# Kernel optimization log

Hardware: AMD Instinct MI355X
Metric: run time of the kernel (lower is better)

The kernel has to match this reference:

```python
import jax, jax.numpy as jnp
import numpy as np

K = 10
NEG_SLOPE = 0.2


def _knn(x, k):
    # x: (B, C, N) -> idx (B, N, k) of k nearest neighbors (smallest sq-dist)
    inner = -2.0 * jnp.einsum('bcn,bcm->bnm', x, x)
    xx = jnp.sum(x * x, axis=1)  # (B, N)
    pd = -xx[:, :, None] - inner - xx[:, None, :]  # negative squared distance
    return jax.lax.top_k(pd, k)[1]


def _gather(xt, idx):
    # xt: (B, N, C), idx: (B, N, k) -> (B, N, k, C)
    return jax.vmap(lambda f, i: f[i])(xt, idx)


def graph_feature(x, k):
    # x: (B, C, N) -> (B, 2C, N, k)
    idx = _knn(x, k)
    xt = jnp.transpose(x, (0, 2, 1))  # (B, N, C)
    feat = _gather(xt, idx)           # (B, N, k, C)
    xc = xt[:, :, None, :]
    out = jnp.concatenate([feat - xc, jnp.broadcast_to(xc, feat.shape)], axis=3)
    return jnp.transpose(out, (0, 3, 1, 2))


def graph_feature1(x, k):
    # knn on first 2 dims (2D coords); x: (B, C, N) -> (B, 2C, N, k)
    idx = _knn(x[:, 0:2, :], k)
    xt = jnp.transpose(x, (0, 2, 1))
    feat = _gather(xt, idx)
    xc = jnp.broadcast_to(xt[:, :, None, :], feat.shape)
    out = jnp.concatenate([feat[..., :2] - xc[..., :2], feat[..., 2:], xc], axis=3)
    return jnp.transpose(out, (0, 3, 1, 2))


def _lrelu(v):
    return jnp.where(v >= 0, v, NEG_SLOPE * v)


def _cbr2(f, W, s, t):
    # 1x1 conv2d + folded-BN + leaky relu; f: (B, C, N, k)
    y = jnp.einsum('oc,bcnk->bonk', W, f)
    return _lrelu(y * s[None, :, None, None] + t[None, :, None, None])


def _cbr1(f, W, s, t):
    # 1x1 conv1d + folded-BN + leaky relu; f: (B, C, N)
    y = jnp.einsum('oc,bcn->bon', W, f)
    return _lrelu(y * s[None, :, None] + t[None, :, None])


def setup_inputs() -> dict:
    key = jax.random.key(0)
    ks = jax.random.split(key, 32)
    B, C, N = 8, 7, 4096
    d = {'x': jax.random.normal(ks[0], (B, C, N), jnp.float32)}
    wshapes = [('W1', (64, 14)), ('W2', (64, 64)), ('W3', (64, 128)), ('W4', (64, 64)),
               ('W5', (64, 128)), ('W6', (256, 192)), ('W7', (512, 448)), ('W8', (128, 1024))]
    for i, (n, s) in enumerate(wshapes):
        d[n] = jax.random.normal(ks[1 + i], s, jnp.float32) * (1.0 / np.sqrt(s[1]))
    bdims = [64, 64, 64, 64, 64, 256, 512, 128]
    for i, c in enumerate(bdims):
        d[f's{i + 1}'] = jax.random.uniform(ks[9 + i], (c,), jnp.float32, 0.5, 1.5)
        d[f't{i + 1}'] = jax.random.normal(ks[17 + i], (c,), jnp.float32) * 0.1
    return d


def reference(x, W1, W2, W3, W4, W5, W6, W7, W8,
              s1, s2, s3, s4, s5, s6, s7, s8,
              t1, t2, t3, t4, t5, t6, t7, t8):
    B, _, N = x.shape
    h = graph_feature1(x, K)              # (B, 14, N, K)
    h = _cbr2(h, W1, s1, t1)
    h = _cbr2(h, W2, s2, t2)
    x1 = h.mean(axis=-1)                  # (B, 64, N)
    h = graph_feature(x1, K)              # (B, 128, N, K)
    h = _cbr2(h, W3, s3, t3)
    h = _cbr2(h, W4, s4, t4)
    x2 = h.mean(axis=-1)
    h = graph_feature(x2, K)
    h = _cbr2(h, W5, s5, t5)
    x3 = h.mean(axis=-1)
    h = jnp.concatenate([x1, x2, x3], axis=1)   # (B, 192, N)
    h = _cbr1(h, W6, s6, t6)                    # (B, 256, N)
    g = h.mean(axis=-1, keepdims=True)          # (B, 256, 1)
    g = jnp.broadcast_to(g, (B, 256, N))
    h = jnp.concatenate([g, x1, x2, x3], axis=1)  # (B, 448, N)
    h = _cbr1(h, W7, s7, t7)                      # (B, 512, N)
    x4 = h.max(axis=-1)
    x5 = h.mean(axis=-1)
    h = jnp.concatenate([x4, x5], axis=1)         # (B, 1024)
    h = h @ W8.T                                  # (B, 128)
    return _lrelu(h * s8[None, :] + t8[None, :])
```

## Files before the change

### kernel.cpp

```cpp
#include <hip/hip_runtime.h>

#define BB 8
#define NN 4096
#define KK 10
#define CAP 24
#define TT 4
typedef unsigned long long u64;
typedef __attribute__((ext_vector_type(8))) short bf16x8;
typedef __attribute__((ext_vector_type(4))) float f32x4;

__device__ __forceinline__ float lrelu(float v){ return v >= 0.f ? v : 0.2f*v; }
__device__ __forceinline__ float bc(float v, int l){
  return __int_as_float(__builtin_amdgcn_readlane(__float_as_int(v), l));
}
__device__ __forceinline__ unsigned fenc(float f){
  unsigned u = __float_as_uint(f);
  return u ^ (((unsigned)((int)u >> 31)) | 0x80000000u);
}
__device__ __forceinline__ float fdec(unsigned e){
  return (e & 0x80000000u) ? __uint_as_float(e & 0x7fffffffu) : __uint_as_float(~e);
}

__global__ __launch_bounds__(256) void prep_k(
    const float* __restrict__ W1, const float* __restrict__ W2, const float* __restrict__ W3,
    const float* __restrict__ W4, const float* __restrict__ W5, const float* __restrict__ W8,
    float* __restrict__ W1T, float* __restrict__ W2T, float* __restrict__ W8T,
    unsigned short* __restrict__ W3dh, unsigned short* __restrict__ W3dl,
    unsigned short* __restrict__ W3qh, unsigned short* __restrict__ W3ql,
    unsigned short* __restrict__ W4h,  unsigned short* __restrict__ W4l,
    unsigned short* __restrict__ W5dh, unsigned short* __restrict__ W5dl,
    unsigned short* __restrict__ W5qh, unsigned short* __restrict__ W5ql)
{
  const int t = blockIdx.x*256 + threadIdx.x;
  const int stride = gridDim.x*256;
  for (int i=t; i<64*14; i+=stride){ int o=i/14, c=i%14; W1T[c*64+o]=W1[i]; }
  for (int i=t; i<64*64; i+=stride){ int o=i>>6, c=i&63; W2T[c*64+o]=W2[i]; }
  for (int i=t; i<128*1024; i+=stride){ int o=i>>10, c=i&1023; W8T[c*128+o]=W8[i]; }
  for (int i=t; i<64*64; i+=stride){
    int o=i>>6, c=i&63;
    float f = W3[o*128 + c];
    unsigned u = __float_as_uint(f);
    W3dh[i] = (unsigned short)(u >> 16);
    float lo = f - __uint_as_float(u & 0xffff0000u);
    W3dl[i] = (unsigned short)(__float_as_uint(lo) >> 16);
  }
  for (int i=t; i<64*64; i+=stride){
    int o=i>>6, c=i&63;
    float f = W3[o*128 + 64 + c];
    unsigned u = __float_as_uint(f);
    W3qh[i] = (unsigned short)(u >> 16);
    float lo = f - __uint_as_float(u & 0xffff0000u);
    W3ql[i] = (unsigned short)(__float_as_uint(lo) >> 16);
  }
  for (int i=t; i<64*64; i+=stride){
    float f = W4[i];
    unsigned u = __float_as_uint(f);
    W4h[i] = (unsigned short)(u >> 16);
    float lo = f - __uint_as_float(u & 0xffff0000u);
    W4l[i] = (unsigned short)(__float_as_uint(lo) >> 16);
  }
  for (int i=t; i<64*64; i+=stride){
    int o=i>>6, c=i&63;
    float f = W5[o*128 + c];
    unsigned u = __float_as_uint(f);
    W5dh[i] = (unsigned short)(u >> 16);
    float lo = f - __uint_as_float(u & 0xffff0000u);
    W5dl[i] = (unsigned short)(__float_as_uint(lo) >> 16);
  }
  for (int i=t; i<64*64; i+=stride){
    int o=i>>6, c=i&63;
    float f = W5[o*128 + 64 + c];
    unsigned u = __float_as_uint(f);
    W5qh[i] = (unsigned short)(u >> 16);
    float lo = f - __uint_as_float(u & 0xffff0000u);
    W5ql[i] = (unsigned short)(__float_as_uint(lo) >> 16);
  }
}

__global__ __launch_bounds__(256) void cvt_k(const float* __restrict__ xin,
    unsigned short* __restrict__ Xh, unsigned short* __restrict__ Xl, float* __restrict__ xx)
{
  const int gid = blockIdx.x*256 + threadIdx.x;
  const int p = gid >> 3, c8 = (gid & 7) << 3;
  const float* src = xin + (size_t)p*64 + c8;
  float fv[8];
  *(float4*)&fv[0] = *(const float4*)(src);
  *(float4*)&fv[4] = *(const float4*)(src + 4);
  unsigned hp[4], lp[4];
  float ssq = 0.f;
  #pragma unroll
  for (int e=0; e<4; e++){
    float f0 = fv[2*e], f1 = fv[2*e+1];
    ssq += f0*f0 + f1*f1;
    unsigned u0 = __float_as_uint(f0), u1 = __float_as_uint(f1);
    hp[e] = (u0 >> 16) | (u1 & 0xffff0000u);
    float l0 = f0 - __uint_as_float(u0 & 0xffff0000u);
    float l1 = f1 - __uint_as_float(u1 & 0xffff0000u);
    lp[e] = (__float_as_uint(l0) >> 16) | (__float_as_uint(l1) & 0xffff0000u);
  }
  *(uint4*)(Xh + (size_t)p*64 + c8) = uint4{hp[0],hp[1],hp[2],hp[3]};
  *(uint4*)(Xl + (size_t)p*64 + c8) = uint4{lp[0],lp[1],lp[2],lp[3]};
  ssq += __shfl_xor(ssq, 1, 64);
  ssq += __shfl_xor(ssq, 2, 64);
  ssq += __shfl_xor(ssq, 4, 64);
  if ((gid & 7) == 0) xx[p] = ssq;
}

__global__ __launch_bounds__(256) void knn2d_k(const float* __restrict__ x, u64* __restrict__ pk)
{
  __shared__ float px[1024], py[1024], pxx[1024];
  __shared__ unsigned cnt[64];
  __shared__ u64 lst[CAP][64];
  const int tid = threadIdx.x;
  const int b  = blockIdx.x >> 8;
  const int qt = (blockIdx.x >> 2) & 63;
  const int h  = blockIdx.x & 3;
  const int q0 = qt*64;
  const int m0g = h*1024;
  const float* xb = x + (size_t)b*7*NN;
  for (int m = tid; m < 1024; m += 256){
    float a = xb[m0g + m], c = xb[NN + m0g + m];
    px[m] = a; py[m] = c; pxx[m] = a*a + c*c;
  }
  if (tid < 64) cnt[tid] = 0;
  __syncthreads();

  const int ty = tid >> 4, tx = tid & 15;
  const int qr = ty*4;
  float qx4[4], qy4[4], q24[4];
  #pragma unroll
  for (int i=0;i<4;i++){
    float a = xb[q0+qr+i], c = xb[NN + q0+qr+i];
    qx4[i] = a; qy4[i] = c; q24[i] = a*a + c*c;
  }

  float bv[4][TT];
  #pragma unroll
  for (int i=0;i<4;i++){
    #pragma unroll
    for (int s=0;s<TT;s++) bv[i][s] = -__builtin_inff();
  }

  for (int ot=0; ot<8; ot++){
    #pragma unroll
    for (int j=0;j<8;j++){
      const int ml = ot*128 + j*16 + tx;
      const float cmx = px[ml], cmy = py[ml], cm2 = pxx[ml];
      #pragma unroll
      for (int i=0;i<4;i++){
        float dot = qx4[i]*cmx + qy4[i]*cmy;
        float v = (-q24[i]) - (-2.f*dot) - cm2;
        float c = v;
        #pragma unroll
        for (int s=0;s<TT;s++){
          float nb = fmaxf(bv[i][s], c);
          c = fminf(bv[i][s], c);
          bv[i][s] = nb;
        }
      }
    }
  }

  float thr[4];
  #pragma unroll
  for (int i=0;i<4;i++){
    float m = 0.f;
    #pragma unroll
    for (int k=0;k<10;k++){
      float hh = bv[i][0];
      m = hh;
      m = fmaxf(m, __shfl_xor(m, 1, 64));
      m = fmaxf(m, __shfl_xor(m, 2, 64));
      m = fmaxf(m, __shfl_xor(m, 4, 64));
      m = fmaxf(m, __shfl_xor(m, 8, 64));
      if (k < 9){
        if (hh == m){
          #pragma unroll
          for (int s=0;s<TT-1;s++) bv[i][s] = bv[i][s+1];
          bv[i][TT-1] = -__builtin_inff();
        }
      }
    }
    thr[i] = m;
  }

  for (int ot=0; ot<8; ot++){
    #pragma unroll
    for (int j=0;j<8;j++){
      const int ml = ot*128 + j*16 + tx;
      const float cmx = px[ml], cmy = py[ml], cm2 = pxx[ml];
// ... 74 lines not shown
  }

  for (int ct=0; ct<16; ct++){
    const int m0 = m0g + ct*64;
    __syncthreads();
    {
      const uint4* sh = (const uint4*)(Xhb + (size_t)(m0+sp)*64 + sc);
      const uint4* sl = (const uint4*)(Xlb + (size_t)(m0+sp)*64 + sc);
      uint4 h0 = sh[0], h1 = sh[1], l0 = sl[0], l1 = sl[1];
      *(uint4*)(&Ch[sp*72 + sc])     = h0;
      *(uint4*)(&Ch[sp*72 + sc + 8]) = h1;
      *(uint4*)(&Cl[sp*72 + sc])     = l0;
      *(uint4*)(&Cl[sp*72 + sc + 8]) = l1;
      if (tid < 64) cxx[tid] = xxb[m0 + tid];
    }
    __syncthreads();

    #pragma unroll
    for (int j=0;j<4;j++){
      const int boff = (j*16 + col)*72 + quad*8;
      bf16x8 Bh0 = *(const bf16x8*)(&Ch[boff]);
      bf16x8 Bh1 = *(const bf16x8*)(&Ch[boff+32]);
      bf16x8 Bl0 = *(const bf16x8*)(&Cl[boff]);
      bf16x8 Bl1 = *(const bf16x8*)(&Cl[boff+32]);
      f32x4 d = {0.f,0.f,0.f,0.f};
      d = __builtin_amdgcn_mfma_f32_16x16x32_bf16(Al0, Bh0, d, 0,0,0);
      d = __builtin_amdgcn_mfma_f32_16x16x32_bf16(Ah0, Bl0, d, 0,0,0);
      d = __builtin_amdgcn_mfma_f32_16x16x32_bf16(Ah0, Bh0, d, 0,0,0);
      d = __builtin_amdgcn_mfma_f32_16x16x32_bf16(Al1, Bh1, d, 0,0,0);
      d = __builtin_amdgcn_mfma_f32_16x16x32_bf16(Ah1, Bl1, d, 0,0,0);
      d = __builtin_amdgcn_mfma_f32_16x16x32_bf16(Ah1, Bh1, d, 0,0,0);

      const float cx = cxx[j*16 + col];
      #pragma unroll
      for (int i=0;i<4;i++){
        float v = (-qx4[i]) - (-2.f*d[i]) - cx;
        float c = v;
        #pragma unroll
        for (int s=0;s<TT;s++){
          float nb = fmaxf(bv[i][s], c);
          c = fminf(bv[i][s], c);
          bv[i][s] = nb;
        }
      }
    }
  }

  float thr[4];
  #pragma unroll
  for (int i=0;i<4;i++){
    float m = 0.f;
    #pragma unroll
    for (int k=0;k<10;k++){
      float hh = bv[i][0];
      m = hh;
      m = fmaxf(m, __shfl_xor(m, 1, 64));
      m = fmaxf(m, __shfl_xor(m, 2, 64));
      m = fmaxf(m, __shfl_xor(m, 4, 64));
      m = fmaxf(m, __shfl_xor(m, 8, 64));
      if (k < 9){
        if (hh == m){
          #pragma unroll
          for (int s=0;s<TT-1;s++) bv[i][s] = bv[i][s+1];
          bv[i][TT-1] = -__builtin_inff();
        }
      }
    }
    thr[i] = m;
  }

  for (int ct=0; ct<16; ct++){
    const int m0 = m0g + ct*64;
    __syncthreads();
    {
      const uint4* sh = (const uint4*)(Xhb + (size_t)(m0+sp)*64 + sc);
      const uint4* sl = (const uint4*)(Xlb + (size_t)(m0+sp)*64 + sc);
      uint4 h0 = sh[0], h1 = sh[1], l0 = sl[0], l1 = sl[1];
      *(uint4*)(&Ch[sp*72 + sc])     = h0;
      *(uint4*)(&Ch[sp*72 + sc + 8]) = h1;
      *(uint4*)(&Cl[sp*72 + sc])     = l0;
      *(uint4*)(&Cl[sp*72 + sc + 8]) = l1;
      if (tid < 64) cxx[tid] = xxb[m0 + tid];
    }
    __syncthreads();

    #pragma unroll
    for (int j=0;j<4;j++){
      const int boff = (j*16 + col)*72 + quad*8;
      bf16x8 Bh0 = *(const bf16x8*)(&Ch[boff]);
      bf16x8 Bh1 = *(const bf16x8*)(&Ch[boff+32]);
      bf16x8 Bl0 = *(const bf16x8*)(&Cl[boff]);
      bf16x8 Bl1 = *(const bf16x8*)(&Cl[boff+32]);
      f32x4 d = {0.f,0.f,0.f,0.f};
      d = __builtin_amdgcn_mfma_f32_16x16x32_bf16(Al0, Bh0, d, 0,0,0);
      d = __builtin_amdgcn_mfma_f32_16x16x32_bf16(Ah0, Bl0, d, 0,0,0);
      d = __builtin_amdgcn_mfma_f32_16x16x32_bf16(Ah0, Bh0, d, 0,0,0);
      d = __builtin_amdgcn_mfma_f32_16x16x32_bf16(Al1, Bh1, d, 0,0,0);
      d = __builtin_amdgcn_mfma_f32_16x16x32_bf16(Ah1, Bl1, d, 0,0,0);
      d = __builtin_amdgcn_mfma_f32_16x16x32_bf16(Ah1, Bh1, d, 0,0,0);

      const int m = m0 + j*16 + col;
      const float cx = cxx[j*16 + col];
      const unsigned mk = ~(unsigned)m;
      #pragma unroll
      for (int i=0;i<4;i++){
        float v = (-qx4[i]) - (-2.f*d[i]) - cx;
        if (v >= thr[i]){
          u64 key = ((u64)fenc(v) << 32) | mk;
          const int r = qr + i;
          unsigned slot = atomicAdd(&cnt[r], 1u);
          if (slot < CAP) lst[slot][r] = key;
        }
      }
    }
  }
  __syncthreads();

  if (tid < 64){
    int n = (int)cnt[tid]; if (n > CAP) n = CAP;
    u64* op = pk + (((size_t)b*NN + q0 + tid)*4 + h)*KK;
    for (int k=0;k<KK;k++){
      u64 best = 0ull; int bi = 0;
      for (int s=0;s<n;s++){
        u64 v2 = lst[s][tid];
        if (v2 > best){ best = v2; bi = s; }
      }
      if (best) lst[bi][tid] = 0ull;
      op[k] = best;
    }
  }
}

__global__ __launch_bounds__(256) void kmerge_k(const u64* __restrict__ pk, int* __restrict__ idxo)
{
  const int q = blockIdx.x*256 + threadIdx.x;
  const u64* A = pk + (size_t)q*(4*KK);
  int* op = idxo + (size_t)q*KK;
  int ia = 0, ib = 0, ic = 0, id = 0;
  #pragma unroll
  for (int k=0;k<KK;k++){
    u64 a  = (ia < KK) ? A[ia]        : 0ull;
    u64 b2 = (ib < KK) ? A[KK + ib]   : 0ull;
    u64 c2 = (ic < KK) ? A[2*KK + ic] : 0ull;
    u64 d2 = (id < KK) ? A[3*KK + id] : 0ull;
    u64 m1 = a >= b2 ? a : b2;  int s1 = a >= b2 ? 0 : 1;
    u64 m2 = c2 >= d2 ? c2 : d2; int s2 = c2 >= d2 ? 2 : 3;
    u64 mm = m1 >= m2 ? m1 : m2; int ss = m1 >= m2 ? s1 : s2;
    op[k] = (int)(~(unsigned)mm);
    if (ss == 0) ia++; else if (ss == 1) ib++; else if (ss == 2) ic++; else id++;
  }
}

__global__ __launch_bounds__(256) void edge1_k(const float* __restrict__ x, const int* __restrict__ idx,
    const float* __restrict__ W1T, const float* __restrict__ W2T,
    const float* __restrict__ s1, const float* __restrict__ t1,
    const float* __restrict__ s2, const float* __restrict__ t2,
    float* __restrict__ x1t)
{
  const int lane = threadIdx.x & 63;
  const int pt = (blockIdx.x << 2) + (threadIdx.x >> 6);
  const int b = pt >> 12, n = pt & 4095;
  const float* xb = x + (size_t)b*7*NN;
  float w1r[14], w2r[64];
  #pragma unroll
  for (int c=0;c<14;c++) w1r[c] = W1T[c*64 + lane];
  #pragma unroll
  for (int c=0;c<64;c++) w2r[c] = W2T[c*64 + lane];
  const float s1o=s1[lane], t1o=t1[lane], s2o=s2[lane], t2o=t2[lane];
  const float xq = (lane < 7) ? xb[lane*NN + n] : 0.f;
  const float xq0 = bc(xq,0), xq1 = bc(xq,1);
  float qy1 = 0.f;
  #pragma unroll
  for (int c=0;c<7;c++) qy1 += w1r[7+c]*bc(xq,c);
  const int* ip = idx + (size_t)pt*KK;
  float acc = 0.f;
  for (int j=0;j<KK;j++){
    const int ij = ip[j];
    const float xg = (lane < 7) ? xb[lane*NN + ij] : 0.f;
    float y1 = qy1;
    y1 += w1r[0]*(bc(xg,0) - xq0);
    y1 += w1r[1]*(bc(xg,1) - xq1);
    #pragma unroll
    for (int c=2;c<7;c++) y1 += w1r[c]*bc(xg,c);
    const float z1 = lrelu(y1*s1o + t1o);
    float p0=0.f,p1=0.f,p2=0.f,p3=0.f;
    #pragma unroll
    for (int c=0;c<64;c+=4){
      p0 += w2r[c+0]*bc(z1,c+0);
      p1 += w2r[c+1]*bc(z1,c+1);
      p2 += w2r[c+2]*bc(z1,c+2);
      p3 += w2r[c+3]*bc(z1,c+3);
    }
    acc += lrelu(((p0+p1)+(p2+p3))*s2o + t2o);
  }
  x1t[(size_t)pt*64 + lane] = acc / 10.f;
}

__global__ __launch_bounds__(256) void edge2_k(const float* __restrict__ x1t, const int* __restrict__ idx,
    const unsigned short* __restrict__ W3dh, const unsigned short* __restrict__ W3dl,
    const unsigned short* __restrict__ W3qh, const unsigned short* __restrict__ W3ql,
    const unsigned short* __restrict__ W4h,  const unsigned short* __restrict__ W4l,
    const float* __restrict__ s3, const float* __restrict__ t3,
    const float* __restrict__ s4, const float* __restrict__ t4,
    float* __restrict__ xout)
{
  __shared__ unsigned short Zh[80*72], Zl[80*72];
  __shared__ unsigned short Qh[16*72], Ql[16*72];
  __shared__ float accf[64*8];
  const int tid = threadIdx.x;
  const size_t p0 = (size_t)blockIdx.x * 8;

  ((float2*)accf)[tid] = float2{0.f, 0.f};

  #pragma unroll
  for (int pass=0; pass<2; ++pass){
    const int col = pass*64 + (tid>>2);
    const int sc16 = (tid&3)*16;
    if (col < 88){
      float dv[16];
      if (col < 80){
        const int p = col/10, j = col - p*10;
        const size_t pt = p0 + p;
        const int bb = (int)(pt >> 12);
        const int ij = idx[pt*KK + j];
        const float* gs = x1t + ((size_t)bb*NN + ij)*64 + sc16;
        const float* qs = x1t + pt*64 + sc16;
        #pragma unroll
        for (int e=0;e<4;e++){
          float4 g4 = *(const float4*)(gs + e*4);
          float4 q4 = *(const float4*)(qs + e*4);
          dv[e*4+0]=g4.x-q4.x; dv[e*4+1]=g4.y-q4.y; dv[e*4+2]=g4.z-q4.z; dv[e*4+3]=g4.w-q4.w;
        }
      } else {
        const int cl = col - 80;
        const float* qs = x1t + (size_t)(p0+cl)*64 + sc16;
        #pragma unroll
        for (int e=0;e<4;e++){
          float4 q4 = *(const float4*)(qs + e*4);
          dv[e*4+0]=q4.x; dv[e*4+1]=q4.y; dv[e*4+2]=q4.z; dv[e*4+3]=q4.w;
        }
      }
      unsigned hp[8], lp[8];
      #pragma unroll
      for (int e=0;e<8;e++){
        float f0 = dv[2*e], f1 = dv[2*e+1];
        unsigned u0 = __float_as_uint(f0), u1 = __float_as_uint(f1);
        hp[e] = (u0 >> 16) | (u1 & 0xffff0000u);
        float l0 = f0 - __uint_as_float(u0 & 0xffff0000u);
        float l1 = f1 - __uint_as_float(u1 & 0xffff0000u);
        lp[e] = (__float_as_uint(l0) >> 16) | (__float_as_uint(l1) & 0xffff0000u);
      }
      if (col < 80){
        *(uint4*)(&Zh[col*72 + sc16])     = uint4{hp[0],hp[1],hp[2],hp[3]};
        *(uint4*)(&Zh[col*72 + sc16 + 8]) = uint4{hp[4],hp[5],hp[6],hp[7]};
        *(uint4*)(&Zl[col*72 + sc16])     = uint4{lp[0],lp[1],lp[2],lp[3]};
        *(uint4*)(&Zl[col*72 + sc16 + 8]) = uint4{lp[4],lp[5],lp[6],lp[7]};
      } else {
        const int cl = col - 80;
        *(uint4*)(&Qh[cl*72 + sc16])     = uint4{hp[0],hp[1],hp[2],hp[3]};
        *(uint4*)(&Qh[cl*72 + sc16 + 8]) = uint4{hp[4],hp[5],hp[6],hp[7]};
        *(uint4*)(&Ql[cl*72 + sc16])     = uint4{lp[0],lp[1],lp[2],lp[3]};
        *(uint4*)(&Ql[cl*72 + sc16 + 8]) = uint4{lp[4],lp[5],lp[6],lp[7]};
      }
    } else if (col < 96){
      const int cl = col - 80;
      const uint4 z{0u,0u,0u,0u};
      *(uint4*)(&Qh[cl*72 + sc16])     = z;
      *(uint4*)(&Qh[cl*72 + sc16 + 8]) = z;
      *(uint4*)(&Ql[cl*72 + sc16])     = z;
      *(uint4*)(&Ql[cl*72 + sc16 + 8]) = z;
    }
  }
  __syncthreads();

  const int lane = tid & 63;
  const int w    = tid >> 6;
  const int colL = lane & 15;
  const int quad = lane >> 4;
  const int arow = (w*16 + colL)*64 + quad*8;

  bf16x8 Adh0 = *(const bf16x8*)(W3dh + arow);
  bf16x8 Adh1 = *(const bf16x8*)(W3dh + arow + 32);
  bf16x8 Adl0 = *(const bf16x8*)(W3dl + arow);
  bf16x8 Adl1 = *(const bf16x8*)(W3dl + arow + 32);

  f32x4 C1[5];
  #pragma unroll
  for (int t=0;t<5;t++){
    const int boff = (t*16 + colL)*72 + quad*8;
    bf16x8 Bh0 = *(const bf16x8*)(&Zh[boff]);
    bf16x8 Bh1 = *(const bf16x8*)(&Zh[boff+32]);
    bf16x8 Bl0 = *(const bf16x8*)(&Zl[boff]);
    bf16x8 Bl1 = *(const bf16x8*)(&Zl[boff+32]);
    f32x4 d = {0.f,0.f,0.f,0.f};
    d = __builtin_amdgcn_mfma_f32_16x16x32_bf16(Adl0, Bh0, d, 0,0,0);
    d = __builtin_amdgcn_mfma_f32_16x16x32_bf16(Adh0, Bl0, d, 0,0,0);
    d = __builtin_amdgcn_mfma_f32_16x16x32_bf16(Adh0, Bh0, d, 0,0,0);
    d = __builtin_amdgcn_mfma_f32_16x16x32_bf16(Adl1, Bh1, d, 0,0,0);
    d = __builtin_amdgcn_mfma_f32_16x16x32_bf16(Adh1, Bl1, d, 0,0,0);
    d = __builtin_amdgcn_mfma_f32_16x16x32_bf16(Adh1, Bh1, d, 0,0,0);
    C1[t] = d;
  }
  f32x4 Cu;
  {
    bf16x8 Aqh0 = *(const bf16x8*)(W3qh + arow);
    bf16x8 Aqh1 = *(const bf16x8*)(W3qh + arow + 32);
    bf16x8 Aql0 = *(const bf16x8*)(W3ql + arow);
    bf16x8 Aql1 = *(const bf16x8*)(W3ql + arow + 32);
    const int boff = colL*72 + quad*8;
    bf16x8 Bh0 = *(const bf16x8*)(&Qh[boff]);
    bf16x8 Bh1 = *(const bf16x8*)(&Qh[boff+32]);
    bf16x8 Bl0 = *(const bf16x8*)(&Ql[boff]);
    bf16x8 Bl1 = *(const bf16x8*)(&Ql[boff+32]);
    f32x4 d = {0.f,0.f,0.f,0.f};
    d = __builtin_amdgcn_mfma_f32_16x16x32_bf16(Aql0, Bh0, d, 0,0,0);
    d = __builtin_amdgcn_mfma_f32_16x16x32_bf16(Aqh0, Bl0, d, 0,0,0);
    d = __builtin_amdgcn_mfma_f32_16x16x32_bf16(Aqh0, Bh0, d, 0,0,0);
    d = __builtin_amdgcn_mfma_f32_16x16x32_bf16(Aql1, Bh1, d, 0,0,0);
    d = __builtin_amdgcn_mfma_f32_16x16x32_bf16(Aqh1, Bl1, d, 0,0,0);
    d = __builtin_amdgcn_mfma_f32_16x16x32_bf16(Aqh1, Bh1, d, 0,0,0);
    Cu = d;
  }

  float s3v[4], t3v[4], s4v[4], t4v[4];
  #pragma unroll
  for (int i=0;i<4;i++){
    const int o = w*16 + quad*4 + i;
    s3v[i]=s3[o]; t3v[i]=t3[o]; s4v[i]=s4[o]; t4v[i]=t4[o];
  }

  __syncthreads();

  #pragma unroll
  for (int t=0;t<5;t++){
    const int gc = t*16 + colL;
    const int p  = gc/10;
    const int srcb = (((lane & 48) | p) << 2);
    float z[4];
    #pragma unroll
    for (int i=0;i<4;i++){
      float ui = __int_as_float(__builtin_amdgcn_ds_bpermute(srcb, __float_as_int(Cu[i])));
      float zp = (C1[t][i] + ui)*s3v[i] + t3v[i];
      z[i] = zp >= 0.f ? zp : 0.2f*zp;
    }
    unsigned u0=__float_as_uint(z[0]), u1=__float_as_uint(z[1]);
    unsigned u2=__float_as_uint(z[2]), u3=__float_as_uint(z[3]);
    unsigned h01 = (u0>>16) | (u1 & 0xffff0000u);
    unsigned h23 = (u2>>16) | (u3 & 0xffff0000u);
// ... 280 lines not shown
{
  const int b = blockIdx.x >> 1;
  const int o = (blockIdx.x & 1)*256 + threadIdx.x;
  const float* wr = W7 + (size_t)o*448;
  const float* gb = gsum + b*256;
  float a0=0.f,a1=0.f,a2=0.f,a3=0.f;
  #pragma unroll 4
  for (int c=0;c<256;c+=4){
    a0 += wr[c+0]*gb[c+0]; a1 += wr[c+1]*gb[c+1];
    a2 += wr[c+2]*gb[c+2]; a3 += wr[c+3]*gb[c+3];
  }
  c7[b*512+o] = ((a0+a1)+(a2+a3)) * (1.f/4096.f);
}

__global__ __launch_bounds__(256) void g3_k(const float* __restrict__ W7,
   const float* __restrict__ x1t, const float* __restrict__ x2t, const float* __restrict__ x3t,
   const float* __restrict__ c7, const float* __restrict__ s7, const float* __restrict__ t7,
   unsigned* __restrict__ x4e, float* __restrict__ x5s)
{
  __shared__ float Wl[16*132];
  __shared__ float Zl[16*260];
  const int tid = threadIdx.x;
  const int rb = blockIdx.x & 3;
  const int nt = (blockIdx.x >> 2) & 15;
  const int b  = blockIdx.x >> 6;
  const int r0 = rb*128;
  const int n0 = nt*256;
  const int ty = tid >> 4, tx = tid & 15;
  float acc[8][16];
  #pragma unroll
  for (int i=0;i<8;i++){
    #pragma unroll
    for (int j=0;j<16;j++) acc[i][j] = 0.f;
  }
  for (int kc=0; kc<12; kc++){
    __syncthreads();
    {
      const int r = tid >> 1, h = tid & 1;
      const float4* wp = (const float4*)(W7 + (size_t)(r0 + r)*448 + 256 + kc*16 + h*8);
      float tmp[8];
      *(float4*)&tmp[0] = wp[0];
      *(float4*)&tmp[4] = wp[1];
      #pragma unroll
      for (int u=0;u<8;u++) Wl[(h*8+u)*132 + r] = tmp[u];
    }
    {
      const float* arr = (kc < 4) ? x1t : (kc < 8) ? x2t : x3t;
      const int chofs = (kc & 3)*16;
      const float4* zp = (const float4*)(arr + ((size_t)(b*NN) + n0 + tid)*64 + chofs);
      float tmp[16];
      *(float4*)&tmp[0]  = zp[0];
      *(float4*)&tmp[4]  = zp[1];
      *(float4*)&tmp[8]  = zp[2];
      *(float4*)&tmp[12] = zp[3];
      #pragma unroll
      for (int u=0;u<16;u++) Zl[u*260 + tid] = tmp[u];
    }
    __syncthreads();
    #pragma unroll 4
    for (int k=0;k<16;k++){
      float wv[8], zv[16];
      *(float4*)&wv[0] = *(const float4*)(&Wl[k*132 + ty*8]);
      *(float4*)&wv[4] = *(const float4*)(&Wl[k*132 + ty*8 + 4]);
      #pragma unroll
      for (int jg=0;jg<4;jg++)
        *(float4*)&zv[jg*4] = *(const float4*)(&Zl[k*260 + jg*64 + tx*4]);
      #pragma unroll
      for (int i=0;i<8;i++){
        #pragma unroll
        for (int j=0;j<16;j++) acc[i][j] += wv[i]*zv[j];
      }
    }
  }
  #pragma unroll
  for (int i=0;i<8;i++){
    const int row = r0 + ty*8 + i;
    const float c7v = c7[b*512 + row];
    const float sv = s7[row], tv = t7[row];
    float mx = -__builtin_inff(), sum = 0.f;
    #pragma unroll
    for (int j=0;j<16;j++){
      float h = lrelu((acc[i][j] + c7v)*sv + tv);
      mx = fmaxf(mx, h); sum += h;
    }
    #pragma unroll
    for (int d=1; d<16; d<<=1){
      sum += __shfl_xor(sum, d, 64);
      mx = fmaxf(mx, __shfl_xor(mx, d, 64));
    }
    if ((tid & 15) == 0){
      atomicAdd(&x5s[b*512 + row], sum);
      atomicMax(&x4e[b*512 + row], fenc(mx));
    }
  }
}

__global__ __launch_bounds__(128) void g4_k(const float* __restrict__ W8T,
  const unsigned* __restrict__ x4e, const float* __restrict__ x5s,
  const float* __restrict__ s8, const float* __restrict__ t8, float* __restrict__ out)
{
  const int b = blockIdx.x, j = threadIdx.x;
  float a0 = 0.f, a1 = 0.f;
  for (int o=0;o<512;o++){
    a0 += W8T[o*128 + j] * fdec(x4e[b*512 + o]);
    a1 += W8T[(512+o)*128 + j] * (x5s[b*512 + o] * (1.f/4096.f));
  }
  const float y = a0 + a1;
  out[b*128 + j] = lrelu(y*s8[j] + t8[j]);
}

extern "C" void kernel_launch(void* const* d_in, const int* in_sizes, int n_in,
                              void* d_out, int out_size, void* d_ws, size_t ws_size,
                              hipStream_t stream) {
  (void)in_sizes; (void)n_in; (void)out_size; (void)ws_size;
  const float* x  = (const float*)d_in[0];
  const float* W1 = (const float*)d_in[1];
  const float* W2 = (const float*)d_in[2];
  const float* W3 = (const float*)d_in[3];
  const float* W4 = (const float*)d_in[4];
  const float* W5 = (const float*)d_in[5];
  const float* W6 = (const float*)d_in[6];
  const float* W7 = (const float*)d_in[7];
  const float* W8 = (const float*)d_in[8];
  const float* s1 = (const float*)d_in[9];   const float* t1 = (const float*)d_in[10];
  const float* s2 = (const float*)d_in[11];  const float* t2 = (const float*)d_in[12];
  const float* s3 = (const float*)d_in[13];  const float* t3 = (const float*)d_in[14];
  const float* s4 = (const float*)d_in[15];  const float* t4 = (const float*)d_in[16];
  const float* s5 = (const float*)d_in[17];  const float* t5 = (const float*)d_in[18];
  const float* s6 = (const float*)d_in[19];  const float* t6 = (const float*)d_in[20];
  const float* s7 = (const float*)d_in[21];  const float* t7 = (const float*)d_in[22];
  const float* s8 = (const float*)d_in[23];  const float* t8 = (const float*)d_in[24];

  char* wsb = (char*)d_ws;
  size_t off = 0;
  auto alloc = [&](size_t bytes)->char* {
    char* p = wsb + off;
    off += (bytes + 255) & ~(size_t)255;
    return p;
  };
  int*      idx1 = (int*)alloc((size_t)BB*NN*KK*4);
  int*      idx2 = (int*)alloc((size_t)BB*NN*KK*4);
  int*      idx3 = (int*)alloc((size_t)BB*NN*KK*4);
  u64*      pkeys= (u64*)alloc((size_t)BB*NN*4*KK*8);
  float*    x1t  = (float*)alloc((size_t)BB*NN*64*4);
  float*    x2t  = (float*)alloc((size_t)BB*NN*64*4);
  float*    x3t  = (float*)alloc((size_t)BB*NN*64*4);
  unsigned short* Xh = (unsigned short*)alloc((size_t)BB*NN*64*2);
  unsigned short* Xl = (unsigned short*)alloc((size_t)BB*NN*64*2);
  float*    xxb  = (float*)alloc((size_t)BB*NN*4);
  float*    gsum = (float*)alloc((size_t)BB*256*4);
  unsigned* x4e  = (unsigned*)alloc((size_t)BB*512*4);
  float*    x5s  = (float*)alloc((size_t)BB*512*4);
  float*    c7   = (float*)alloc((size_t)BB*512*4);
  float*    W1T  = (float*)alloc(14*64*4);
  float*    W2T  = (float*)alloc(64*64*4);
  float*    W8T  = (float*)alloc(1024*128*4);
  unsigned short* W3dh = (unsigned short*)alloc(64*64*2);
  unsigned short* W3dl = (unsigned short*)alloc(64*64*2);
  unsigned short* W3qh = (unsigned short*)alloc(64*64*2);
  unsigned short* W3ql = (unsigned short*)alloc(64*64*2);
  unsigned short* W4h  = (unsigned short*)alloc(64*64*2);
  unsigned short* W4l  = (unsigned short*)alloc(64*64*2);
  unsigned short* W5dh = (unsigned short*)alloc(64*64*2);
  unsigned short* W5dl = (unsigned short*)alloc(64*64*2);
  unsigned short* W5qh = (unsigned short*)alloc(64*64*2);
  unsigned short* W5ql = (unsigned short*)alloc(64*64*2);

  prep_k<<<64,256,0,stream>>>(W1,W2,W3,W4,W5,W8, W1T,W2T,W8T,
                              W3dh,W3dl,W3qh,W3ql,W4h,W4l, W5dh,W5dl,W5qh,W5ql);
  knn2d_k<<<BB*64*4,256,0,stream>>>(x, pkeys);
  kmerge_k<<<BB*NN/256,256,0,stream>>>(pkeys, idx1);
  edge1_k<<<BB*NN/4,256,0,stream>>>(x, idx1, W1T, W2T, s1,t1,s2,t2, x1t);
  cvt_k<<<BB*NN*8/256,256,0,stream>>>(x1t, Xh, Xl, xxb);
  knn64_k<<<BB*64*4,256,0,stream>>>(Xh, Xl, xxb, pkeys);
  kmerge_k<<<BB*NN/256,256,0,stream>>>(pkeys, idx2);
  edge2_k<<<BB*NN/8,256,0,stream>>>(x1t, idx2, W3dh,W3dl,W3qh,W3ql,W4h,W4l, s3,t3,s4,t4, x2t);
  cvt_k<<<BB*NN*8/256,256,0,stream>>>(x2t, Xh, Xl, xxb);
  knn64_k<<<BB*64*4,256,0,stream>>>(Xh, Xl, xxb, pkeys);
  kmerge_k<<<BB*NN/256,256,0,stream>>>(pkeys, idx3);
  edge3_k<<<BB*NN/8,256,0,stream>>>(x2t, idx3, W5dh,W5dl,W5qh,W5ql, s5,t5, x3t);
  hipMemsetAsync(gsum, 0, (size_t)BB*256*4 + (size_t)BB*512*4*2, stream);
  g1_k<<<256,256,0,stream>>>(W6, x1t,x2t,x3t, s6,t6, gsum);
  g2_k<<<16,256,0,stream>>>(W7, gsum, c7);
  g3_k<<<512,256,0,stream>>>(W7, x1t,x2t,x3t, c7, s7,t7, x4e, x5s);
  g4_k<<<BB,128,0,stream>>>(W8T, x4e, x5s, s8,t8, (float*)d_out);
}
```

Measured before the change: 1.129 ms.

## Rewrite edge1 kernel to use split-bf16 MFMA for both 1x1 convs

Replaces the per-wavefront scalar FMA plus readlane broadcast implementation of the first edge-conv stage with a block that handles 8 points (80 edges). Edge features go to shared memory as hi/lo bf16 pairs, and both layers run on 16x16x32 bf16 MFMA using three products per step to approximate fp32 accuracy. The neighbour mean is reduced through shared-memory atomics. This is meant to remove the long serial readlane/FMA chain, at the cost of extra split-conversion work, zero padding of K from 14 to 32, and LDS atomics.

```diff
diff --git a/kernel.cpp b/kernel.cpp
--- a/kernel.cpp
+++ b/kernel.cpp
@@ -10,9 +10,6 @@
 typedef __attribute__((ext_vector_type(4))) float f32x4;
 
 __device__ __forceinline__ float lrelu(float v){ return v >= 0.f ? v : 0.2f*v; }
-__device__ __forceinline__ float bc(float v, int l){
-  return __int_as_float(__builtin_amdgcn_readlane(__float_as_int(v), l));
-}
 __device__ __forceinline__ unsigned fenc(float f){
   unsigned u = __float_as_uint(f);
   return u ^ (((unsigned)((int)u >> 31)) | 0x80000000u);
@@ -24,7 +21,9 @@
 __global__ __launch_bounds__(256) void prep_k(
     const float* __restrict__ W1, const float* __restrict__ W2, const float* __restrict__ W3,
     const float* __restrict__ W4, const float* __restrict__ W5, const float* __restrict__ W8,
-    float* __restrict__ W1T, float* __restrict__ W2T, float* __restrict__ W8T,
+    float* __restrict__ W8T,
+    unsigned short* __restrict__ W1h,  unsigned short* __restrict__ W1l,
+    unsigned short* __restrict__ W2h,  unsigned short* __restrict__ W2l,
     unsigned short* __restrict__ W3dh, unsigned short* __restrict__ W3dl,
     unsigned short* __restrict__ W3qh, unsigned short* __restrict__ W3ql,
     unsigned short* __restrict__ W4h,  unsigned short* __restrict__ W4l,
@@ -33,9 +32,22 @@
 {
   const int t = blockIdx.x*256 + threadIdx.x;
   const int stride = gridDim.x*256;
-  for (int i=t; i<64*14; i+=stride){ int o=i/14, c=i%14; W1T[c*64+o]=W1[i]; }
-  for (int i=t; i<64*64; i+=stride){ int o=i>>6, c=i&63; W2T[c*64+o]=W2[i]; }
   for (int i=t; i<128*1024; i+=stride){ int o=i>>10, c=i&1023; W8T[c*128+o]=W8[i]; }
+  for (int i=t; i<64*32; i+=stride){
+    int o=i>>5, c=i&31;
+    float f = (c < 14) ? W1[o*14 + c] : 0.f;
+    unsigned u = __float_as_uint(f);
+    W1h[i] = (unsigned short)(u >> 16);
+    float lo = f - __uint_as_float(u & 0xffff0000u);
+    W1l[i] = (unsigned short)(__float_as_uint(lo) >> 16);
+  }
+  for (int i=t; i<64*64; i+=stride){
+    float f = W2[i];
+    unsigned u = __float_as_uint(f);
+    W2h[i] = (unsigned short)(u >> 16);
+    float lo = f - __uint_as_float(u & 0xffff0000u);
+    W2l[i] = (unsigned short)(__float_as_uint(lo) >> 16);
+  }
   for (int i=t; i<64*64; i+=stride){
     int o=i>>6, c=i&63;
     float f = W3[o*128 + c];
@@ -416,48 +428,151 @@
 }
 
 __global__ __launch_bounds__(256) void edge1_k(const float* __restrict__ x, const int* __restrict__ idx,
-    const float* __restrict__ W1T, const float* __restrict__ W2T,
+    const unsigned short* __restrict__ W1h, const unsigned short* __restrict__ W1l,
+    const unsigned short* __restrict__ W2h, const unsigned short* __restrict__ W2l,
     const float* __restrict__ s1, const float* __restrict__ t1,
     const float* __restrict__ s2, const float* __restrict__ t2,
     float* __restrict__ x1t)
 {
-  const int lane = threadIdx.x & 63;
-  const int pt = (blockIdx.x << 2) + (threadIdx.x >> 6);
-  const int b = pt >> 12, n = pt & 4095;
-  const float* xb = x + (size_t)b*7*NN;
-  float w1r[14], w2r[64];
-  #pragma unroll
-  for (int c=0;c<14;c++) w1r[c] = W1T[c*64 + lane];
-  #pragma unroll
-  for (int c=0;c<64;c++) w2r[c] = W2T[c*64 + lane];
-  const float s1o=s1[lane], t1o=t1[lane], s2o=s2[lane], t2o=t2[lane];
-  const float xq = (lane < 7) ? xb[lane*NN + n] : 0.f;
-  const float xq0 = bc(xq,0), xq1 = bc(xq,1);
-  float qy1 = 0.f;
-  #pragma unroll
-  for (int c=0;c<7;c++) qy1 += w1r[7+c]*bc(xq,c);
-  const int* ip = idx + (size_t)pt*KK;
-  float acc = 0.f;
-  for (int j=0;j<KK;j++){
-    const int ij = ip[j];
-    const float xg = (lane < 7) ? xb[lane*NN + ij] : 0.f;
-    float y1 = qy1;
-    y1 += w1r[0]*(bc(xg,0) - xq0);
-    y1 += w1r[1]*(bc(xg,1) - xq1);
-    #pragma unroll
-    for (int c=2;c<7;c++) y1 += w1r[c]*bc(xg,c);
-    const float z1 = lrelu(y1*s1o + t1o);
-    float p0=0.f,p1=0.f,p2=0.f,p3=0.f;
-    #pragma unroll
-    for (int c=0;c<64;c+=4){
-      p0 += w2r[c+0]*bc(z1,c+0);
-      p1 += w2r[c+1]*bc(z1,c+1);
-      p2 += w2r[c+2]*bc(z1,c+2);
-      p3 += w2r[c+3]*bc(z1,c+3);
-    }
-    acc += lrelu(((p0+p1)+(p2+p3))*s2o + t2o);
-  }
-  x1t[(size_t)pt*64 + lane] = acc / 10.f;
+  __shared__ unsigned short Fh[80*36], Fl[80*36];
+  __shared__ unsigned short Zh[80*72], Zl[80*72];
+  __shared__ float accf[64*8];
+  const int tid = threadIdx.x;
+  const size_t p0 = (size_t)blockIdx.x * 8;
+
+  ((float2*)accf)[tid] = float2{0.f, 0.f};
+
+  if (tid < 80){
+    const int p = tid/10, j = tid - p*10;
+    const size_t pt = p0 + p;
+    const int bb = (int)(pt >> 12);
+    const int n = (int)(pt & 4095);
+    const int ij = idx[pt*KK + j];
+    const float* xb = x + (size_t)bb*7*NN;
+    float f[16];
+    const float q0v = xb[n], q1v = xb[NN + n];
+    f[0] = xb[ij] - q0v;
+    f[1] = xb[NN + ij] - q1v;
+    #pragma unroll
+    for (int c=2;c<7;c++) f[c] = xb[c*NN + ij];
+    f[7] = q0v; f[8] = q1v;
+    #pragma unroll
+    for (int c=2;c<7;c++) f[7+c] = xb[c*NN + n];
+    f[14] = 0.f; f[15] = 0.f;
+    unsigned hp[8], lp[8];
+    #pragma unroll
+    for (int e=0;e<8;e++){
+      float a0 = f[2*e], a1 = f[2*e+1];
+      unsigned u0 = __float_as_uint(a0), u1 = __float_as_uint(a1);
+      hp[e] = (u0 >> 16) | (u1 & 0xffff0000u);
+      float l0 = a0 - __uint_as_float(u0 & 0xffff0000u);
+      float l1 = a1 - __uint_as_float(u1 & 0xffff0000u);
+      lp[e] = (__float_as_uint(l0) >> 16) | (__float_as_uint(l1) & 0xffff0000u);
+    }
+    const uint4 z{0u,0u,0u,0u};
+    *(uint4*)(&Fh[tid*36])      = uint4{hp[0],hp[1],hp[2],hp[3]};
+    *(uint4*)(&Fh[tid*36 + 8])  = uint4{hp[4],hp[5],hp[6],hp[7]};
+    *(uint4*)(&Fh[tid*36 + 16]) = z;
+    *(uint4*)(&Fh[tid*36 + 24]) = z;
+    *(uint4*)(&Fl[tid*36])      = uint4{lp[0],lp[1],lp[2],lp[3]};
+    *(uint4*)(&Fl[tid*36 + 8])  = uint4{lp[4],lp[5],lp[6],lp[7]};
+    *(uint4*)(&Fl[tid*36 + 16]) = z;
+    *(uint4*)(&Fl[tid*36 + 24]) = z;
+  }
+  __syncthreads();
+
+  const int lane = tid & 63;
+  const int w    = tid >> 6;
+  const int colL = lane & 15;
+  const int quad = lane >> 4;
+
+  const int arow1 = (w*16 + colL)*32 + quad*8;
+  bf16x8 A1h = *(const bf16x8*)(W1h + arow1);
+  bf16x8 A1l = *(const bf16x8*)(W1l + arow1);
+
+  f32x4 C1[5];
+  #pragma unroll
+  for (int t=0;t<5;t++){
+    const int boff = (t*16 + colL)*36 + quad*8;
+    bf16x8 Bh = *(const bf16x8*)(&Fh[boff]);
+    bf16x8 Bl = *(const bf16x8*)(&Fl[boff]);
+    f32x4 d = {0.f,0.f,0.f,0.f};
+    d = __builtin_amdgcn_mfma_f32_16x16x32_bf16(A1l, Bh, d, 0,0,0);
+    d = __builtin_amdgcn_mfma_f32_16x16x32_bf16(A1h, Bl, d, 0,0,0);
+    d = __builtin_amdgcn_mfma_f32_16x16x32_bf16(A1h, Bh, d, 0,0,0);
+    C1[t] = d;
+  }
+
+  float s1v[4], t1v[4], s2v[4], t2v[4];
+  #pragma unroll
+  for (int i=0;i<4;i++){
+    const int o = w*16 + quad*4 + i;
+    s1v[i]=s1[o]; t1v[i]=t1[o]; s2v[i]=s2[o]; t2v[i]=t2[o];
+  }
+
+  #pragma unroll
+  for (int t=0;t<5;t++){
+    const int gc = t*16 + colL;
+    float z[4];
+    #pragma unroll
+    for (int i=0;i<4;i++){
+      float zp = C1[t][i]*s1v[i] + t1v[i];
+      z[i] = zp >= 0.f ? zp : 0.2f*zp;
+    }
+    unsigned u0=__float_as_uint(z[0]), u1=__float_as_uint(z[1]);
+    unsigned u2=__float_as_uint(z[2]), u3=__float_as_uint(z[3]);
+    unsigned h01 = (u0>>16) | (u1 & 0xffff0000u);
+    unsigned h23 = (u2>>16) | (u3 & 0xffff0000u);
+    float l0 = z[0]-__uint_as_float(u0&0xffff0000u);
+    float l1 = z[1]-__uint_as_float(u1&0xffff0000u);
+    float l2 = z[2]-__uint_as_float(u2&0xffff0000u);
+    float l3 = z[3]-__uint_as_float(u3&0xffff0000u);
+    unsigned l01 = (__float_as_uint(l0)>>16) | (__float_as_uint(l1)&0xffff0000u);
+    unsigned l23 = (__float_as_uint(l2)>>16) | (__float_as_uint(l3)&0xffff0000u);
+    const int rb = w*16 + quad*4;
+    *(uint2*)(&Zh[gc*72 + rb]) = uint2{h01,h23};
+    *(uint2*)(&Zl[gc*72 + rb]) = uint2{l01,l23};
+  }
+  __syncthreads();
+
+  const int arow = (w*16 + colL)*64 + quad*8;
+  bf16x8 A2h0 = *(const bf16x8*)(W2h + arow);
+  bf16x8 A2h1 = *(const bf16x8*)(W2h + arow + 32);
+  bf16x8 A2l0 = *(const bf16x8*)(W2l + arow);
+  bf16x8 A2l1 = *(const bf16x8*)(W2l + arow + 32);
+  #pragma unroll
+  for (int t=0;t<5;t++){
+    const int boff = (t*16 + colL)*72 + quad*8;
+    bf16x8 Bh0 = *(const bf16x8*)(&Zh[boff]);
+    bf16x8 Bh1 = *(const bf16x8*)(&Zh[boff+32]);
+    bf16x8 Bl0 = *(const bf16x8*)(&Zl[boff]);
+    bf16x8 Bl1 = *(const bf16x8*)(&Zl[boff+32]);
+    f32x4 d = {0.f,0.f,0.f,0.f};
+    d = __builtin_amdgcn_mfma_f32_16x16x32_bf16(A2l0, Bh0, d, 0,0,0);
+    d = __builtin_amdgcn_mfma_f32_16x16x32_bf16(A2h0, Bl0, d, 0,0,0);
+    d = __builtin_amdgcn_mfma_f32_16x16x32_bf16(A2h0, Bh0, d, 0,0,0);
+    d = __builtin_amdgcn_mfma_f32_16x16x32_bf16(A2l1, Bh1, d, 0,0,0);
+    d = __builtin_amdgcn_mfma_f32_16x16x32_bf16(A2h1, Bl1, d, 0,0,0);
+    d = __builtin_amdgcn_mfma_f32_16x16x32_bf16(A2h1, Bh1, d, 0,0,0);
+    const int gc = t*16 + colL;
+    const int p  = gc/10;
+    #pragma unroll
+    for (int i=0;i<4;i++){
+      float v = d[i]*s2v[i] + t2v[i];
+      v = v >= 0.f ? v : 0.2f*v;
+      atomicAdd(&accf[(w*16 + quad*4 + i)*8 + p], v);
+    }
+  }
+  __syncthreads();
+
+  {
+    const int o = tid & 63;
+    #pragma unroll
+    for (int g=0; g<2; ++g){
+      const int p = (tid>>6) + g*4;
+      x1t[(p0+p)*64 + o] = accf[o*8+p] / 10.f;
+    }
+  }
 }
 
 __global__ __launch_bounds__(256) void edge2_k(const float* __restrict__ x1t, const int* __restrict__ idx,
@@ -1044,9 +1159,11 @@
   unsigned* x4e  = (unsigned*)alloc((size_t)BB*512*4);
   float*    x5s  = (float*)alloc((size_t)BB*512*4);
   float*    c7   = (float*)alloc((size_t)BB*512*4);
-  float*    W1T  = (float*)alloc(14*64*4);
-  float*    W2T  = (float*)alloc(64*64*4);
   float*    W8T  = (float*)alloc(1024*128*4);
+  unsigned short* W1h  = (unsigned short*)alloc(64*32*2);
+  unsigned short* W1l  = (unsigned short*)alloc(64*32*2);
+  unsigned short* W2h  = (unsigned short*)alloc(64*64*2);
+  unsigned short* W2l  = (unsigned short*)alloc(64*64*2);
   unsigned short* W3dh = (unsigned short*)alloc(64*64*2);
   unsigned short* W3dl = (unsigned short*)alloc(64*64*2);
   unsigned short* W3qh = (unsigned short*)alloc(64*64*2);
@@ -1058,11 +1175,12 @@
   unsigned short* W5qh = (unsigned short*)alloc(64*64*2);
   unsigned short* W5ql = (unsigned short*)alloc(64*64*2);
 
-  prep_k<<<64,256,0,stream>>>(W1,W2,W3,W4,W5,W8, W1T,W2T,W8T,
+  prep_k<<<64,256,0,stream>>>(W1,W2,W3,W4,W5,W8, W8T,
+                              W1h,W1l,W2h,W2l,
                               W3dh,W3dl,W3qh,W3ql,W4h,W4l, W5dh,W5dl,W5qh,W5ql);
   knn2d_k<<<BB*64*4,256,0,stream>>>(x, pkeys);
   kmerge_k<<<BB*NN/256,256,0,stream>>>(pkeys, idx1);
-  edge1_k<<<BB*NN/4,256,0,stream>>>(x, idx1, W1T, W2T, s1,t1,s2,t2, x1t);
+  edge1_k<<<BB*NN/8,256,0,stream>>>(x, idx1, W1h,W1l,W2h,W2l, s1,t1,s2,t2, x1t);
   cvt_k<<<BB*NN*8/256,256,0,stream>>>(x1t, Xh, Xl, xxb);
   knn64_k<<<BB*64*4,256,0,stream>>>(Xh, Xl, xxb, pkeys);
   kmerge_k<<<BB*NN/256,256,0,stream>>>(pkeys, idx2);
```

Result: slower. 1.194 ms (+5.8%).
